# Optimization experiments

Hardware: AMD Instinct MI355X
Metric: run time of the kernel (lower is better)

Reference implementation:

```python
import jax, jax.numpy as jnp
import numpy as np

NUM_REP = 3

def setup_inputs() -> dict:
    N, E, DIM, R2, L, B, NEG = 20000, 100000, 32, 100, 4, 4, 32
    ks = jax.random.split(jax.random.key(0), 12)
    # all negatives in a row share the same head (required by the model's assert)
    h = jax.random.randint(ks[0], (B, 1), 0, N)
    t = jax.random.randint(ks[1], (B, NEG), 0, N)
    batch = jnp.stack([jnp.broadcast_to(h, (B, NEG)), t], axis=-1)  # [B,NEG,2]
    edge_index = jax.random.randint(ks[2], (2, E), 0, N)
    edge_type = jax.random.randint(ks[3], (E,), 0, R2)
    edge_attr = 0.1 * jax.random.normal(ks[4], (E, DIM), jnp.float32)
    start_query = jax.random.normal(ks[5], (NUM_REP, DIM), jnp.float32)
    W_rel = jax.random.normal(ks[6], (L, DIM, R2 * DIM), jnp.float32) * (DIM ** -0.5)
    b_rel = jnp.zeros((L, R2 * DIM), jnp.float32)
    W_lin = jax.random.normal(ks[7], (L, 2 * DIM, DIM), jnp.float32) * ((2 * DIM) ** -0.5)
    b_lin = jnp.zeros((L, DIM), jnp.float32)
    W_mlp1 = jax.random.normal(ks[8], (DIM, DIM), jnp.float32) * (DIM ** -0.5)
    b_mlp1 = jnp.zeros((DIM,), jnp.float32)
    W_mlp2 = jax.random.normal(ks[9], (DIM, DIM), jnp.float32) * (DIM ** -0.5)
    b_mlp2 = jnp.zeros((DIM,), jnp.float32)
    return {"batch": batch, "edge_index": edge_index, "edge_type": edge_type,
            "edge_attr": edge_attr, "num_nodes": N, "start_query": start_query,
            "W_rel": W_rel, "b_rel": b_rel, "W_lin": W_lin, "b_lin": b_lin,
            "W_mlp1": W_mlp1, "b_mlp1": b_mlp1, "W_mlp2": W_mlp2, "b_mlp2": b_mlp2}

def reference(batch, edge_index, edge_type, edge_attr, num_nodes, start_query,
              W_rel, b_rel, W_lin, b_lin, W_mlp1, b_mlp1, W_mlp2, b_mlp2):
    B, num_neg, _ = batch.shape
    N = int(num_nodes)
    dim = start_query.shape[1]
    L = W_rel.shape[0]
    bs = NUM_REP * B
    batch_full = jnp.tile(batch, (NUM_REP, 1, 1))            # [bs, neg, 2]
    query_idx = jnp.repeat(jnp.arange(NUM_REP), B)           # [bs]
    h_index, t_index = batch_full[..., 0], batch_full[..., 1]
    # negative_sample_to_tail (no-op when heads are constant per row, as built)
    is_t_neg = jnp.all(h_index == h_index[:, :1], axis=-1, keepdims=True)
    h_index, t_index = (jnp.where(is_t_neg, h_index, t_index),
                        jnp.where(is_t_neg, t_index, h_index))
    h0 = h_index[:, 0]
    q = start_query[query_idx]                               # [bs, dim]
    rows = jnp.arange(bs)
    boundary = jnp.zeros((bs, N, dim), q.dtype).at[rows, h0].add(q)
    pb = jnp.zeros((bs, N), q.dtype).at[rows, h0].set(1.0)   # path boundary
    src, dst = edge_index[0], edge_index[1]
    x = boundary
    for l in range(L):
        # dependent per-query relation embeddings: [bs, 2R, dim]
        rel = (q @ W_rel[l] + b_rel[l]).reshape(bs, -1, dim)
        rel_e = rel[:, edge_type] + edge_attr[None]          # [bs, E, dim]
        msg = x[:, src] * rel_e                              # distmult message
        # sum aggregation; boundary acts as the self-loop message
        agg = jnp.zeros((bs, N, dim), x.dtype).at[:, dst].add(msg) + boundary
        x = jax.nn.relu(jnp.concatenate([x, agg], axis=-1) @ W_lin[l] + b_lin[l])
        # reachability propagation of the path boundary (scatter-max)
        pb = jnp.maximum(pb, jnp.zeros((bs, N), pb.dtype).at[:, dst].max(pb[:, src]))
    feat_t = x[rows[:, None], t_index]                       # [bs, neg, dim]
    feat = feat_t.reshape(NUM_REP, B, num_neg, dim).mean(0)  # mean over reps
    features = jax.nn.relu(feat @ W_mlp1 + b_mlp1) @ W_mlp2 + b_mlp2
    pb_t = pb[rows[:, None], t_index][..., None]             # [bs, neg, 1]
    path_boundary = pb_t.reshape(NUM_REP, B, num_neg, 1).max(0)
    return features, path_boundary
```

## Files before the change

### kernel.cpp

```cpp
#include <hip/hip_runtime.h>

#define N_NODES 20000
#define N_EDGES 100000
#define DIM 32
#define R2 100
#define NLAYERS 4
#define BATCH 4
#define NEG 32
#define NREP 3
#define BS (NREP * BATCH)
#define RELDIM (R2 * DIM)
#define NCHUNK (N_NODES / 32)
#define GRID_LAYER (((NCHUNK + 7) / 8) * BS * 8)

#define XO_A 0
#define XO_B (XO_A + (size_t)BS * N_NODES * DIM)
#define PBO_A (XO_B + (size_t)BS * N_NODES * DIM)
#define PBO_B (PBO_A + (size_t)BS * N_NODES)
#define RELO (PBO_B + (size_t)BS * N_NODES)
#define QO (RELO + (size_t)NLAYERS * BS * RELDIM)
#define FLOAT_TOTAL (QO + (size_t)BS * DIM)

#define IO_H0 0
#define IO_TIDX (IO_H0 + BS)
#define IO_COUNTS (IO_TIDX + BS * NEG)
#define IO_OFF (IO_COUNTS + N_NODES)
#define IO_CURSOR (IO_OFF + N_NODES + 1)
#define IO_PERM (IO_CURSOR + N_NODES)
#define INT_TOTAL (IO_PERM + N_EDGES)

__global__ void k_init(const int* __restrict__ batch,
                       const float* __restrict__ start_query,
                       float* __restrict__ q, int* __restrict__ h0,
                       int* __restrict__ t_idx) {
    int r = threadIdx.x;
    if (r >= BS) return;
    int b = r % BATCH, rep = r / BATCH;
    int h00 = batch[(b * NEG + 0) * 2 + 0];
    bool is_t_neg = true;
    for (int j = 0; j < NEG; j++)
        if (batch[(b * NEG + j) * 2 + 0] != h00) { is_t_neg = false; break; }
    int hsel = is_t_neg ? 0 : 1;
    int h0v = batch[(b * NEG + 0) * 2 + hsel];
    h0[r] = h0v;
    for (int j = 0; j < NEG; j++)
        t_idx[r * NEG + j] = batch[(b * NEG + j) * 2 + (1 - hsel)];
    for (int d = 0; d < DIM; d++) q[r * DIM + d] = start_query[rep * DIM + d];
}

__global__ void k_count(const int* __restrict__ dst, int* __restrict__ counts) {
    int e = blockIdx.x * blockDim.x + threadIdx.x;
    if (e < N_EDGES) atomicAdd(&counts[dst[e]], 1);
}

__global__ void k_scan(const int* __restrict__ counts, int* __restrict__ off,
                       int* __restrict__ cursor) {
    __shared__ int sd[1024];
    int t = threadIdx.x;
    const int CH = (N_NODES + 1023) / 1024;
    int base = t * CH;
    int sum = 0;
    for (int i = 0; i < CH; i++) {
        int idx = base + i;
        if (idx < N_NODES) sum += counts[idx];
    }
    sd[t] = sum;
    __syncthreads();
    for (int o = 1; o < 1024; o <<= 1) {
        int v = (t >= o) ? sd[t - o] : 0;
        __syncthreads();
        sd[t] += v;
        __syncthreads();
    }
    int excl = sd[t] - sum;
    int run = excl;
    for (int i = 0; i < CH; i++) {
        int idx = base + i;
        if (idx < N_NODES) {
            off[idx] = run;
            cursor[idx] = run;
            run += counts[idx];
        }
    }
    if (t == 1023) off[N_NODES] = sd[1023];
}

__global__ void k_place(const int* __restrict__ dst, int* __restrict__ cursor,
                        int* __restrict__ perm) {
    int e = blockIdx.x * blockDim.x + threadIdx.x;
    if (e < N_EDGES) {
        int p = atomicAdd(&cursor[dst[e]], 1);
        perm[p] = e;
    }
}

__global__ void k_rel_all(const float* __restrict__ q, const float* __restrict__ W_rel,
                          const float* __restrict__ b_rel, float* __restrict__ rel) {
    int idx = blockIdx.x * blockDim.x + threadIdx.x;
    if (idx >= NLAYERS * BS * RELDIM) return;
    int l = idx / (BS * RELDIM);
    int rem = idx - l * (BS * RELDIM);
    int r = rem / RELDIM;
    int c = rem - r * RELDIM;
    const float* W = W_rel + (size_t)l * DIM * RELDIM;
    float acc = b_rel[l * RELDIM + c];
    #pragma unroll
    for (int k = 0; k < DIM; k++) acc += q[r * DIM + k] * W[(size_t)k * RELDIM + c];
    rel[idx] = acc;
}

template <bool L0>
__launch_bounds__(256)
__global__ void k_layer(const float* __restrict__ x_old, const float* __restrict__ pb_old,
                        const float* __restrict__ rel_l, const float* __restrict__ edge_attr,
                        const int* __restrict__ src, const int* __restrict__ etype,
                        const int* __restrict__ off, const int* __restrict__ perm,
                        const int* __restrict__ h0, const float* __restrict__ q,
                        const float* __restrict__ W_lin_l, const float* __restrict__ b_lin_l,
                        float* __restrict__ x_new, float* __restrict__ pb_new) {
    int p = blockIdx.x;
    int cgrp = (p & 7) + 8 * ((p >> 3) / BS);
    int r = (p >> 3) % BS;
    if (cgrp >= NCHUNK) return;

    __shared__ float sW[64 * DIM];
    __shared__ float sB[DIM];
    __shared__ float sIn[32 * 68];

    for (int i = threadIdx.x; i < 64 * DIM; i += 256) sW[i] = W_lin_l[i];
    if (threadIdx.x < DIM) sB[threadIdx.x] = b_lin_l[threadIdx.x];

    const int g = threadIdx.x >> 3;
    const int l = threadIdx.x & 7;
    const int n = cgrp * 32 + g;
    const size_t idx = (size_t)r * N_NODES + n;
    const int h0r = h0[r];

    const float4 q4 = *(const float4*)(q + r * DIM + l * 4);
    float4 xr4, ag4 = make_float4(0.f, 0.f, 0.f, 0.f);
    float pbm;
    if (L0) {
        xr4 = (n == h0r) ? q4 : make_float4(0.f, 0.f, 0.f, 0.f);
        pbm = (n == h0r) ? 1.f : 0.f;
    } else {
        xr4 = *(const float4*)(x_old + idx * DIM + l * 4);
        pbm = pb_old[idx];
    }

    const int s0 = off[n], s1 = off[n + 1];
    const float* xbase = x_old + (size_t)r * N_NODES * DIM;
    const float* pbbase = pb_old + (size_t)r * N_NODES;
    const float* relr = rel_l + (size_t)r * RELDIM;
    for (int k = s0; k < s1; k++) {
        int e = perm[k];
        int s = src[e];
        if (L0) {
            if (s == h0r) {
                int et = etype[e];
                float4 rl = *(const float4*)(relr + (size_t)et * DIM + l * 4);
                float4 ea = *(const float4*)(edge_attr + (size_t)e * DIM + l * 4);
                ag4.x += q4.x * (rl.x + ea.x);
                ag4.y += q4.y * (rl.y + ea.y);
                ag4.z += q4.z * (rl.z + ea.z);
                ag4.w += q4.w * (rl.w + ea.w);
                pbm = 1.f;
            }
        } else {
            int et = etype[e];
            float4 xs = *(const float4*)(xbase + (size_t)s * DIM + l * 4);
            float4 rl = *(const float4*)(relr + (size_t)et * DIM + l * 4);
            float4 ea = *(const float4*)(edge_attr + (size_t)e * DIM + l * 4);
            ag4.x += xs.x * (rl.x + ea.x);
            ag4.y += xs.y * (rl.y + ea.y);
            ag4.z += xs.z * (rl.z + ea.z);
            ag4.w += xs.w * (rl.w + ea.w);
            pbm = fmaxf(pbm, pbbase[s]);
        }
    }
    if (n == h0r) {
        ag4.x += q4.x; ag4.y += q4.y; ag4.z += q4.z; ag4.w += q4.w;
    }

    float* srow = sIn + g * 68;
    *(float4*)(srow + l * 4) = xr4;
    *(float4*)(srow + 32 + l * 4) = ag4;
    __syncthreads();

    float4 acc = *(const float4*)(sB + l * 4);
    #pragma unroll
    for (int k4 = 0; k4 < 16; k4++) {
        float4 v = *(const float4*)(srow + k4 * 4);
        const float* wb = sW + (k4 * 4) * DIM + l * 4;
        float4 w0 = *(const float4*)(wb);
        float4 w1 = *(const float4*)(wb + DIM);
        float4 w2 = *(const float4*)(wb + 2 * DIM);
        float4 w3 = *(const float4*)(wb + 3 * DIM);
        acc.x += v.x * w0.x + v.y * w1.x + v.z * w2.x + v.w * w3.x;
        acc.y += v.x * w0.y + v.y * w1.y + v.z * w2.y + v.w * w3.y;
        acc.z += v.x * w0.z + v.y * w1.z + v.z * w2.z + v.w * w3.z;
        acc.w += v.x * w0.w + v.y * w1.w + v.z * w2.w + v.w * w3.w;
    }
    acc.x = fmaxf(acc.x, 0.f);
    acc.y = fmaxf(acc.y, 0.f);
    acc.z = fmaxf(acc.z, 0.f);
    acc.w = fmaxf(acc.w, 0.f);
    *(float4*)(x_new + idx * DIM + l * 4) = acc;
    if (l == 0) pb_new[idx] = pbm;
}

__launch_bounds__(1024)
__global__ void k_final(const float* __restrict__ x, const float* __restrict__ pb,
                        const int* __restrict__ t_idx,
                        const float* __restrict__ W1, const float* __restrict__ b1,
                        const float* __restrict__ W2, const float* __restrict__ b2,
                        float* __restrict__ out) {
    __shared__ float sW1[DIM * DIM];
    __shared__ float sW2[DIM * DIM];
    __shared__ float sfeat[BATCH * NEG * DIM];
    __shared__ float shid[BATCH * NEG * DIM];
    const int t = threadIdx.x;
    const int NPAIR = BATCH * NEG;

    for (int i = t; i < DIM * DIM; i += 1024) { sW1[i] = W1[i]; sW2[i] = W2[i]; }

    for (int i = t; i < NPAIR * DIM; i += 1024) {
        int pair = i >> 5;
        int d = i & 31;
        int b = pair >> 5;
        int tt = t_idx[pair];
        float s = 0.f;
        #pragma unroll
        for (int rep = 0; rep < NREP; rep++)
            s += x[((size_t)(rep * BATCH + b) * N_NODES + tt) * DIM + d];
        sfeat[i] = s * (1.f / 3.f);
    }
    __syncthreads();

    for (int i = t; i < NPAIR * DIM; i += 1024) {
        int pair = i >> 5;
        int jj = i & 31;
        float a = b1[jj];
        #pragma unroll
        for (int k = 0; k < DIM; k++)
            a += sfeat[pair * DIM + k] * sW1[k * DIM + jj];
        shid[i] = fmaxf(a, 0.f);
    }
    __syncthreads();

    for (int i = t; i < NPAIR * DIM; i += 1024) {
        int pair = i >> 5;
        int jj = i & 31;
        float a = b2[jj];
        #pragma unroll
        for (int k = 0; k < DIM; k++)
            a += shid[pair * DIM + k] * sW2[k * DIM + jj];
        out[i] = a;
    }

    if (t < NPAIR) {
        int b = t >> 5;
        int tt = t_idx[t];
        float pm = 0.f;
        #pragma unroll
        for (int rep = 0; rep < NREP; rep++)
            pm = fmaxf(pm, pb[(size_t)(rep * BATCH + b) * N_NODES + tt]);
        out[NPAIR * DIM + t] = pm;
    }
}

extern "C" void kernel_launch(void* const* d_in, const int* in_sizes, int n_in,
                              void* d_out, int out_size, void* d_ws, size_t ws_size,
                              hipStream_t stream) {
    const int* batch = (const int*)d_in[0];
    const int* edge_index = (const int*)d_in[1];
    const int* edge_type = (const int*)d_in[2];
    const float* edge_attr = (const float*)d_in[3];
    const float* start_query = (const float*)d_in[5];
    const float* W_rel = (const float*)d_in[6];
    const float* b_rel = (const float*)d_in[7];
    const float* W_lin = (const float*)d_in[8];
    const float* b_lin = (const float*)d_in[9];
    const float* W_mlp1 = (const float*)d_in[10];
    const float* b_mlp1 = (const float*)d_in[11];
    const float* W_mlp2 = (const float*)d_in[12];
    const float* b_mlp2 = (const float*)d_in[13];

    float* wf = (float*)d_ws;
    int* wi = (int*)(wf + FLOAT_TOTAL);
    size_t need = FLOAT_TOTAL * sizeof(float) + INT_TOTAL * sizeof(int);
    if (ws_size < need) return;

    float* x_a = wf + XO_A;
    float* x_b = wf + XO_B;
    float* pb_a = wf + PBO_A;
    float* pb_b = wf + PBO_B;
    float* rel = wf + RELO;
    float* q = wf + QO;
    int* h0 = wi + IO_H0;
    int* t_idx = wi + IO_TIDX;
    int* counts = wi + IO_COUNTS;
    int* off = wi + IO_OFF;
    int* cursor = wi + IO_CURSOR;
    int* perm = wi + IO_PERM;

    const int* src = edge_index;
    const int* dst = edge_index + N_EDGES;

    hipMemsetAsync(counts, 0, (size_t)N_NODES * sizeof(int), stream);

    k_init<<<1, 64, 0, stream>>>(batch, start_query, q, h0, t_idx);

    int eb = (N_EDGES + 255) / 256;
    k_count<<<eb, 256, 0, stream>>>(dst, counts);
    k_scan<<<1, 1024, 0, stream>>>(counts, off, cursor);
    k_place<<<eb, 256, 0, stream>>>(dst, cursor, perm);

    int relb = (NLAYERS * BS * RELDIM + 255) / 256;
    k_rel_all<<<relb, 256, 0, stream>>>(q, W_rel, b_rel, rel);

    k_layer<true><<<GRID_LAYER, 256, 0, stream>>>(
        x_a, pb_a, rel, edge_attr, src, edge_type, off, perm, h0, q,
        W_lin, b_lin, x_a, pb_a);

    float* x_cur = x_a;
    float* x_nxt = x_b;
    float* pb_cur = pb_a;
    float* pb_nxt = pb_b;
    for (int l = 1; l < NLAYERS; l++) {
        k_layer<false><<<GRID_LAYER, 256, 0, stream>>>(
            x_cur, pb_cur, rel + (size_t)l * BS * RELDIM, edge_attr, src, edge_type,
            off, perm, h0, q,
            W_lin + (size_t)l * 64 * DIM, b_lin + (size_t)l * DIM,
            x_nxt, pb_nxt);
        float* tx = x_cur; x_cur = x_nxt; x_nxt = tx;
        float* tp = pb_cur; pb_cur = pb_nxt; pb_nxt = tp;
    }

    k_final<<<1, 1024, 0, stream>>>(x_cur, pb_cur, t_idx, W_mlp1, b_mlp1, W_mlp2, b_mlp2,
                                    (float*)d_out);
}
```

Before: 394.8 us.

## Interleave query batch dimension innermost in node features and relation tables

Changes x, pb and rel layouts from [bs][node][dim] to [node][bs][dim] (and rel to [etype][bs][dim]). Each block now handles 4 nodes across all 12 queries, so the 96 threads of a node share the same edge list and read contiguous 12x32 rows per source node. This is meant to coalesce the gather traffic and reuse perm/src/etype/edge_attr loads across queries. The cost is larger 384-thread blocks and a bigger shared staging buffer.

```diff
diff --git a/kernel.cpp b/kernel.cpp
--- a/kernel.cpp
+++ b/kernel.cpp
@@ -10,15 +10,18 @@
 #define NREP 3
 #define BS (NREP * BATCH)
 #define RELDIM (R2 * DIM)
-#define NCHUNK (N_NODES / 32)
-#define GRID_LAYER (((NCHUNK + 7) / 8) * BS * 8)
+
+#define NPB 4
+#define TPN 96
+#define LBLK (NPB * TPN)
+#define GRID_LAYER (N_NODES / NPB)
 
 #define XO_A 0
-#define XO_B (XO_A + (size_t)BS * N_NODES * DIM)
-#define PBO_A (XO_B + (size_t)BS * N_NODES * DIM)
-#define PBO_B (PBO_A + (size_t)BS * N_NODES)
-#define RELO (PBO_B + (size_t)BS * N_NODES)
-#define QO (RELO + (size_t)NLAYERS * BS * RELDIM)
+#define XO_B (XO_A + (size_t)N_NODES * BS * DIM)
+#define PBO_A (XO_B + (size_t)N_NODES * BS * DIM)
+#define PBO_B (PBO_A + (size_t)N_NODES * BS)
+#define RELO (PBO_B + (size_t)N_NODES * BS)
+#define QO (RELO + (size_t)NLAYERS * R2 * BS * DIM)
 #define FLOAT_TOTAL (QO + (size_t)BS * DIM)
 
 #define IO_H0 0
@@ -97,11 +100,12 @@
 __global__ void k_rel_all(const float* __restrict__ q, const float* __restrict__ W_rel,
                           const float* __restrict__ b_rel, float* __restrict__ rel) {
     int idx = blockIdx.x * blockDim.x + threadIdx.x;
-    if (idx >= NLAYERS * BS * RELDIM) return;
-    int l = idx / (BS * RELDIM);
-    int rem = idx - l * (BS * RELDIM);
-    int r = rem / RELDIM;
-    int c = rem - r * RELDIM;
+    if (idx >= NLAYERS * R2 * BS * DIM) return;
+    int d = idx & 31;
+    int r = (idx >> 5) % BS;
+    int et = (idx / (BS * DIM)) % R2;
+    int l = idx / (R2 * BS * DIM);
+    int c = et * DIM + d;
     const float* W = W_rel + (size_t)l * DIM * RELDIM;
     float acc = b_rel[l * RELDIM + c];
     #pragma unroll
@@ -110,7 +114,7 @@
 }
 
 template <bool L0>
-__launch_bounds__(256)
+__launch_bounds__(LBLK)
 __global__ void k_layer(const float* __restrict__ x_old, const float* __restrict__ pb_old,
                         const float* __restrict__ rel_l, const float* __restrict__ edge_attr,
                         const int* __restrict__ src, const int* __restrict__ etype,
@@ -118,46 +122,40 @@
                         const int* __restrict__ h0, const float* __restrict__ q,
                         const float* __restrict__ W_lin_l, const float* __restrict__ b_lin_l,
                         float* __restrict__ x_new, float* __restrict__ pb_new) {
-    int p = blockIdx.x;
-    int cgrp = (p & 7) + 8 * ((p >> 3) / BS);
-    int r = (p >> 3) % BS;
-    if (cgrp >= NCHUNK) return;
-
     __shared__ float sW[64 * DIM];
     __shared__ float sB[DIM];
-    __shared__ float sIn[32 * 68];
-
-    for (int i = threadIdx.x; i < 64 * DIM; i += 256) sW[i] = W_lin_l[i];
+    __shared__ float sIn[NPB * BS * 68];
+
+    for (int i = threadIdx.x; i < 64 * DIM; i += LBLK) sW[i] = W_lin_l[i];
     if (threadIdx.x < DIM) sB[threadIdx.x] = b_lin_l[threadIdx.x];
 
-    const int g = threadIdx.x >> 3;
-    const int l = threadIdx.x & 7;
-    const int n = cgrp * 32 + g;
-    const size_t idx = (size_t)r * N_NODES + n;
+    const int gi = threadIdx.x / TPN;
+    const int t = threadIdx.x % TPN;
+    const int r = t >> 3;
+    const int l = t & 7;
+    const int n = blockIdx.x * NPB + gi;
+
     const int h0r = h0[r];
-
     const float4 q4 = *(const float4*)(q + r * DIM + l * 4);
+
     float4 xr4, ag4 = make_float4(0.f, 0.f, 0.f, 0.f);
     float pbm;
     if (L0) {
         xr4 = (n == h0r) ? q4 : make_float4(0.f, 0.f, 0.f, 0.f);
         pbm = (n == h0r) ? 1.f : 0.f;
     } else {
-        xr4 = *(const float4*)(x_old + idx * DIM + l * 4);
-        pbm = pb_old[idx];
+        xr4 = *(const float4*)(x_old + ((size_t)n * BS + r) * DIM + l * 4);
+        pbm = pb_old[n * BS + r];
     }
 
     const int s0 = off[n], s1 = off[n + 1];
-    const float* xbase = x_old + (size_t)r * N_NODES * DIM;
-    const float* pbbase = pb_old + (size_t)r * N_NODES;
-    const float* relr = rel_l + (size_t)r * RELDIM;
     for (int k = s0; k < s1; k++) {
         int e = perm[k];
         int s = src[e];
         if (L0) {
             if (s == h0r) {
                 int et = etype[e];
-                float4 rl = *(const float4*)(relr + (size_t)et * DIM + l * 4);
+                float4 rl = *(const float4*)(rel_l + ((size_t)et * BS + r) * DIM + l * 4);
                 float4 ea = *(const float4*)(edge_attr + (size_t)e * DIM + l * 4);
                 ag4.x += q4.x * (rl.x + ea.x);
                 ag4.y += q4.y * (rl.y + ea.y);
@@ -167,21 +165,21 @@
             }
         } else {
             int et = etype[e];
-            float4 xs = *(const float4*)(xbase + (size_t)s * DIM + l * 4);
-            float4 rl = *(const float4*)(relr + (size_t)et * DIM + l * 4);
+            float4 xs = *(const float4*)(x_old + ((size_t)s * BS + r) * DIM + l * 4);
+            float4 rl = *(const float4*)(rel_l + ((size_t)et * BS + r) * DIM + l * 4);
             float4 ea = *(const float4*)(edge_attr + (size_t)e * DIM + l * 4);
             ag4.x += xs.x * (rl.x + ea.x);
             ag4.y += xs.y * (rl.y + ea.y);
             ag4.z += xs.z * (rl.z + ea.z);
             ag4.w += xs.w * (rl.w + ea.w);
-            pbm = fmaxf(pbm, pbbase[s]);
+            pbm = fmaxf(pbm, pb_old[s * BS + r]);
         }
     }
     if (n == h0r) {
         ag4.x += q4.x; ag4.y += q4.y; ag4.z += q4.z; ag4.w += q4.w;
     }
 
-    float* srow = sIn + g * 68;
+    float* srow = sIn + (gi * BS + r) * 68;
     *(float4*)(srow + l * 4) = xr4;
     *(float4*)(srow + 32 + l * 4) = ag4;
     __syncthreads();
@@ -204,8 +202,8 @@
     acc.y = fmaxf(acc.y, 0.f);
     acc.z = fmaxf(acc.z, 0.f);
     acc.w = fmaxf(acc.w, 0.f);
-    *(float4*)(x_new + idx * DIM + l * 4) = acc;
-    if (l == 0) pb_new[idx] = pbm;
+    *(float4*)(x_new + ((size_t)n * BS + r) * DIM + l * 4) = acc;
+    if (l == 0) pb_new[n * BS + r] = pbm;
 }
 
 __launch_bounds__(1024)
@@ -231,7 +229,7 @@
         float s = 0.f;
         #pragma unroll
         for (int rep = 0; rep < NREP; rep++)
-            s += x[((size_t)(rep * BATCH + b) * N_NODES + tt) * DIM + d];
+            s += x[((size_t)tt * BS + rep * BATCH + b) * DIM + d];
         sfeat[i] = s * (1.f / 3.f);
     }
     __syncthreads();
@@ -263,7 +261,7 @@
         float pm = 0.f;
         #pragma unroll
         for (int rep = 0; rep < NREP; rep++)
-            pm = fmaxf(pm, pb[(size_t)(rep * BATCH + b) * N_NODES + tt]);
+            pm = fmaxf(pm, pb[(size_t)tt * BS + rep * BATCH + b]);
         out[NPAIR * DIM + t] = pm;
     }
 }
@@ -315,10 +313,10 @@
     k_scan<<<1, 1024, 0, stream>>>(counts, off, cursor);
     k_place<<<eb, 256, 0, stream>>>(dst, cursor, perm);
 
-    int relb = (NLAYERS * BS * RELDIM + 255) / 256;
+    int relb = (NLAYERS * R2 * BS * DIM + 255) / 256;
     k_rel_all<<<relb, 256, 0, stream>>>(q, W_rel, b_rel, rel);
 
-    k_layer<true><<<GRID_LAYER, 256, 0, stream>>>(
+    k_layer<true><<<GRID_LAYER, LBLK, 0, stream>>>(
         x_a, pb_a, rel, edge_attr, src, edge_type, off, perm, h0, q,
         W_lin, b_lin, x_a, pb_a);
 
@@ -327,8 +325,8 @@
     float* pb_cur = pb_a;
     float* pb_nxt = pb_b;
     for (int l = 1; l < NLAYERS; l++) {
-        k_layer<false><<<GRID_LAYER, 256, 0, stream>>>(
-            x_cur, pb_cur, rel + (size_t)l * BS * RELDIM, edge_attr, src, edge_type,
+        k_layer<false><<<GRID_LAYER, LBLK, 0, stream>>>(
+            x_cur, pb_cur, rel + (size_t)l * R2 * BS * DIM, edge_attr, src, edge_type,
             off, perm, h0, q,
             W_lin + (size_t)l * 64 * DIM, b_lin + (size_t)l * DIM,
             x_nxt, pb_nxt);
```

Result: faster. 376.3 us (-4.7%).
